# Kernel optimization log

Measured on AMD Instinct MI355X. Metric: run time of the kernel, lower is better.

Reference implementation:

```python
import jax, jax.numpy as jnp
import numpy as np

B, N, C, H = 2, 2048, 768, 12
D = C // H  # head dim = 64


def _rotate_half(x):
    d2 = x.shape[-1] // 2
    x1, x2 = x[..., :d2], x[..., d2:]
    return jnp.concatenate([-x2, x1], axis=-1)


def _apply_rope(x, sin, cos):
    # x: [B,H,N,D], sin/cos: [N,D] -> broadcast over (B,H)
    return x * cos[None, None] + _rotate_half(x) * sin[None, None]


def setup_inputs() -> dict:
    key = jax.random.key(0)
    ks = jax.random.split(key, 7)
    x = jax.random.normal(ks[0], (B, N, C), dtype=jnp.float32)
    sin_spatial = jax.random.normal(ks[1], (N, D), dtype=jnp.float32)
    cos_spatial = jax.random.normal(ks[2], (N, D), dtype=jnp.float32)
    s = 1.0 / np.sqrt(C)
    W_qkv = jax.random.uniform(ks[3], (C, 3 * C), jnp.float32, -s, s)
    b_qkv = jax.random.uniform(ks[4], (3 * C,), jnp.float32, -s, s)
    W_out = jax.random.uniform(ks[5], (C, C), jnp.float32, -s, s)
    b_out = jax.random.uniform(ks[6], (C,), jnp.float32, -s, s)
    return {"x": x, "sin_spatial": sin_spatial, "cos_spatial": cos_spatial,
            "W_qkv": W_qkv, "b_qkv": b_qkv, "W_out": W_out, "b_out": b_out}


def reference(x, sin_spatial, cos_spatial, W_qkv, b_qkv, W_out, b_out):
    qkv = x @ W_qkv + b_qkv                       # [B,N,3C]
    qkv = qkv.reshape(B, N, 3, H, D).transpose(2, 0, 3, 1, 4)  # [3,B,H,N,D]
    q, k, v = qkv[0], qkv[1], qkv[2]
    q = _apply_rope(q, sin_spatial, cos_spatial)
    k = _apply_rope(k, sin_spatial, cos_spatial)
    att = jnp.einsum('bhqd,bhkd->bhqk', q, k) * (D ** -0.5)
    att = jax.nn.softmax(att, axis=-1)            # dropout is identity (eval)
    y = jnp.einsum('bhqk,bhkd->bhqd', att, v)     # [B,H,N,D]
    y = y.transpose(0, 2, 1, 3).reshape(B, N, C)
    return y @ W_out + b_out
```

## Files before the change

### kernel.cpp

```cpp
#include <hip/hip_runtime.h>
#include <hip/hip_bf16.h>

#define BB 2
#define NN 2048
#define CC 768
#define HH 12
#define DD 64
#define MM 4096
#define N3 2304

typedef __attribute__((ext_vector_type(8))) short bf16x8;
typedef __attribute__((ext_vector_type(4))) float f32x4;

#define QSCALE 0.18033688011112043f


__device__ __forceinline__ unsigned short f2bf(float f) {
    union { float f; unsigned u; } v; v.f = f;
    unsigned r = v.u + 0x7FFFu + ((v.u >> 16) & 1u);
    return (unsigned short)(r >> 16);
}

__device__ __forceinline__ short f2bf_rn(float f) {
    union { __hip_bfloat16 h; short s; } v;
    v.h = __float2bfloat16(f);
    return v.s;
}

__device__ __forceinline__ float exp2_hw(float x) {
    float r;
    asm("v_exp_f32 %0, %1" : "=v"(r) : "v"(x));
    return r;
}

__device__ __forceinline__ bf16x8 ld_frag16(const unsigned short* p) {
    bf16x8 r;
    __builtin_memcpy(&r, p, 16);
    return r;
}

__device__ __forceinline__ void gload16(const unsigned short* g, unsigned short* l) {
    __builtin_amdgcn_global_load_lds(
        (const __attribute__((address_space(1))) void*)g,
        (__attribute__((address_space(3))) void*)l,
        16, 0, 0);
}

__global__ void k_cvt(const float* __restrict__ s, unsigned short* __restrict__ d, int n4) {
    int i = blockIdx.x * blockDim.x + threadIdx.x;
    int st = gridDim.x * blockDim.x;
    for (; i < n4; i += st) {
        float4 v = ((const float4*)s)[i];
        ushort4 o;
        o.x = f2bf(v.x); o.y = f2bf(v.y); o.z = f2bf(v.z); o.w = f2bf(v.w);
        int f = i * 4;
        int dst = (f & ~31) + ((i & 3) << 3) + (((i >> 2) & 1) << 2);
        *(ushort4*)(d + dst) = o;
    }
}

__global__ void k_cvtT(const float* __restrict__ s, unsigned short* __restrict__ d,
                       int R, int Cc) {
    __shared__ unsigned short t[64][72];
    const int c0 = blockIdx.x * 64, r0 = blockIdx.y * 64;
    const int tr = threadIdx.x >> 4;
    const int tc = (threadIdx.x & 15) * 4;
#pragma unroll
    for (int i = 0; i < 4; i++) {
        int r = tr + i * 16;
        float4 v = *(const float4*)(s + (size_t)(r0 + r) * Cc + c0 + tc);
        t[tc + 0][r] = f2bf(v.x);
        t[tc + 1][r] = f2bf(v.y);
        t[tc + 2][r] = f2bf(v.z);
        t[tc + 3][r] = f2bf(v.w);
    }
    __syncthreads();
    const int wr = threadIdx.x >> 2;
    const int wc = (threadIdx.x & 3) * 16;
    unsigned short* drow = d + (size_t)(c0 + wr) * R + r0;
#pragma unroll
    for (int g = 0; g < 4; g++) {
        int k4 = wc + g * 4;
        int o = k4 & 31;
        int p = (((o & 15) >> 2) << 3) + (((o >> 4) & 1) << 2);
        ushort4 v4 = *(ushort4*)&t[wr][k4];
        *(ushort4*)(drow + (k4 & ~31) + p) = v4;
    }
}

__launch_bounds__(256)
__global__ void k_qkv(const unsigned short* __restrict__ xb,
                      const unsigned short* __restrict__ wt,
                      const float* __restrict__ bias,
                      const float* __restrict__ sinp,
                      const float* __restrict__ cosp,
                      unsigned short* __restrict__ qws,
                      unsigned short* __restrict__ kws,
                      unsigned short* __restrict__ vws) {
    __shared__ unsigned short As[2][128 * 32];
    __shared__ unsigned short Bs[2][64 * 32];
    const int tid = threadIdx.x;
    const int lane = tid & 63, w = tid >> 6;
    const int ql = lane & 15, lg = lane >> 4;
    const int row0 = blockIdx.x * 128;
    const int j0 = blockIdx.y * 64;

    f32x4 acc[2][4];
#pragma unroll
    for (int a = 0; a < 2; a++)
#pragma unroll
        for (int b = 0; b < 4; b++) acc[a][b] = f32x4{0.f, 0.f, 0.f, 0.f};

    const int sr = lane >> 2;
    const int sc = (lane & 3) * 8;

    auto stage = [&](int bi, int k0) {
#pragma unroll
        for (int c = 0; c < 2; c++) {
            int j = w * 2 + c;
            gload16(xb + (size_t)(row0 + j * 16 + sr) * CC + k0 + sc, &As[bi][j * 512]);
        }
        gload16(wt + (size_t)(j0 + w * 16 + sr) * CC + k0 + sc, &Bs[bi][w * 512]);
    };

    stage(0, 0);
    __syncthreads();

    int bufi = 0;
    for (int k0 = 0; k0 < CC; k0 += 32) {
        if (k0 + 32 < CC) stage(bufi ^ 1, k0 + 32);
        bf16x8 af[2], bfr[4];
#pragma unroll
        for (int fr = 0; fr < 2; fr++)
            af[fr] = ld_frag16(&As[bufi][(w * 32 + fr * 16 + ql) * 32 + lg * 8]);
#pragma unroll
        for (int fn = 0; fn < 4; fn++)
            bfr[fn] = ld_frag16(&Bs[bufi][(fn * 16 + ql) * 32 + lg * 8]);
#pragma unroll
        for (int fr = 0; fr < 2; fr++)
#pragma unroll
            for (int fn = 0; fn < 4; fn++)
                acc[fr][fn] = __builtin_amdgcn_mfma_f32_16x16x32_bf16(af[fr], bfr[fn], acc[fr][fn], 0, 0, 0);
        __syncthreads();
        bufi ^= 1;
    }

    float vals[2][4][4];
#pragma unroll
    for (int fr = 0; fr < 2; fr++)
#pragma unroll
        for (int fn = 0; fn < 4; fn++) {
            float bj = bias[j0 + fn * 16 + ql];
#pragma unroll
            for (int r = 0; r < 4; r++) vals[fr][fn][r] = acc[fr][fn][r] + bj;
        }
    const int t = j0 / CC;
    const int h = (j0 % CC) >> 6;
    if (t < 2) {
        unsigned short* outp = (t == 0) ? qws : kws;
        const float qs = (t == 0) ? QSCALE : 1.0f;
#pragma unroll
        for (int fr = 0; fr < 2; fr++)
#pragma unroll
            for (int r = 0; r < 4; r++) {
                int m = row0 + w * 32 + fr * 16 + lg * 4 + r;
                int b = m >> 11, n = m & (NN - 1);
#pragma unroll
                for (int fn = 0; fn < 4; fn++) {
                    int d = fn * 16 + ql;
                    float cv = cosp[n * DD + d], sv = sinp[n * DD + d];
                    float other = vals[fr][fn ^ 2][r];
                    float rv = (vals[fr][fn][r] * cv + ((fn < 2) ? -other : other) * sv) * qs;
                    int dcol = (fn >> 1) * 32 + (ql >> 2) * 8 + (fn & 1) * 4 + (ql & 3);
                    outp[((size_t)(b * HH + h) * NN + n) * DD + dcol] = f2bf(rv);
                }
            }
    } else {
#pragma unroll
        for (int fr = 0; fr < 2; fr++)
#pragma unroll
            for (int r = 0; r < 4; r++) {
                int m = row0 + w * 32 + fr * 16 + lg * 4 + r;
                int b = m >> 11, n = m & (NN - 1);
                int ncol = (n & ~31) + lg * 8 + (fr & 1) * 4 + r;
#pragma unroll
                for (int fn = 0; fn < 4; fn++) {
                    int d = fn * 16 + ql;
                    vws[((size_t)(b * HH + h) * DD + d) * NN + ncol] = f2bf(vals[fr][fn][r]);
                }
            }
    }
}

template <int SPLITK>
__launch_bounds__(128)
__global__ void k_attn_t(const unsigned short* __restrict__ qws,
                         const unsigned short* __restrict__ kws,
                         const unsigned short* __restrict__ vws,
                         unsigned short* __restrict__ yws,
                         float* __restrict__ pA,
                         float* __restrict__ pm,
                         float* __restrict__ pl) {
    __shared__ unsigned short Ks[2][64][72];
    __shared__ unsigned short Vs[2][64][72];
    const int tid = threadIdx.x;
    const int lane = tid & 63, w = tid >> 6;
    const int ql = lane & 15, lg = lane >> 4;
    const int d0 = blockIdx.x;
    int bh, qb, kh;
    if (SPLITK) {
        bh = (d0 & 7) + 8 * (d0 >> 9);
        qb = (d0 >> 3) & 31;
        kh = (d0 >> 8) & 1;
    } else {
        bh = (d0 & 7) + 8 * (d0 >> 8);
        qb = (d0 >> 3) & 31;
        kh = 0;
    }
    const int qw = qb * 64 + w * 32;
    const unsigned short* Qp = qws + (size_t)bh * NN * DD;
    const unsigned short* Kp = kws + (size_t)bh * NN * DD;
    const unsigned short* Vp = vws + (size_t)bh * DD * NN;

    bf16x8 qf[2][2];
#pragma unroll
    for (int fn = 0; fn < 2; fn++)
#pragma unroll
        for (int kb = 0; kb < 2; kb++)
            qf[fn][kb] = ld_frag16(Qp + (size_t)(qw + fn * 16 + ql) * DD + kb * 32 + lg * 8);

    f32x4 oacc[4][2];
#pragma unroll
    for (int a = 0; a < 4; a++)
#pragma unroll
        for (int b = 0; b < 2; b++) oacc[a][b] = f32x4{0.f, 0.f, 0.f, 0.f};
    float mrun[2] = {-1e30f, -1e30f}, lrun[2] = {0.f, 0.f};

    const int srow = tid >> 1;
    const int shalf = (tid & 1) * 32;
    const int kt0 = SPLITK ? kh * 16 : 0;
    const int NT = SPLITK ? 16 : NN / 64;

#pragma unroll
    for (int j = 0; j < 4; j++) {
        *(uint4*)&Ks[0][srow][shalf + j * 8] = *(const uint4*)(Kp + (size_t)(kt0 * 64 + srow) * DD + shalf + j * 8);
        *(uint4*)&Vs[0][srow][shalf + j * 8] = *(const uint4*)(Vp + (size_t)srow * NN + kt0 * 64 + shalf + j * 8);
    }
    __syncthreads();

    int cur = 0;
    for (int t = 0; t < NT; t++) {
        const int kt = kt0 + t;
        uint4 kn[4], vn[4];
        const bool hasn = (t + 1 < NT);
        if (hasn) {
#pragma unroll
            for (int j = 0; j < 4; j++) {
                kn[j] = *(const uint4*)(Kp + (size_t)((kt + 1) * 64 + srow) * DD + shalf + j * 8);
                vn[j] = *(const uint4*)(Vp + (size_t)srow * NN + (kt + 1) * 64 + shalf + j * 8);
            }
        }
        const unsigned short (*Kc)[72] = Ks[cur];
        const unsigned short (*Vc)[72] = Vs[cur];

        f32x4 sacc[4][2];
#pragma unroll
        for (int a = 0; a < 4; a++)
#pragma unroll
            for (int b = 0; b < 2; b++) sacc[a][b] = f32x4{0.f, 0.f, 0.f, 0.f};
        __builtin_amdgcn_s_setprio(1);
#pragma unroll
        for (int kb = 0; kb < 2; kb++) {
            bf16x8 kf[4];
#pragma unroll
            for (int fr = 0; fr < 4; fr++)
                kf[fr] = ld_frag16(&Kc[fr * 16 + ql][kb * 32 + lg * 8]);
#pragma unroll
            for (int fr = 0; fr < 4; fr++)
#pragma unroll
                for (int fn = 0; fn < 2; fn++)
                    sacc[fr][fn] = __builtin_amdgcn_mfma_f32_16x16x32_bf16(kf[fr], qf[fn][kb], sacc[fr][fn], 0, 0, 0);
        }
        __builtin_amdgcn_s_setprio(0);

        bf16x8 pB[2][2];
#pragma unroll
        for (int fn = 0; fn < 2; fn++) {
            float ma = fmaxf(fmaxf(sacc[0][fn][0], sacc[0][fn][1]), fmaxf(sacc[0][fn][2], sacc[0][fn][3]));
            float mb = fmaxf(fmaxf(sacc[1][fn][0], sacc[1][fn][1]), fmaxf(sacc[1][fn][2], sacc[1][fn][3]));
            float mc = fmaxf(fmaxf(sacc[2][fn][0], sacc[2][fn][1]), fmaxf(sacc[2][fn][2], sacc[2][fn][3]));
            float md = fmaxf(fmaxf(sacc[3][fn][0], sacc[3][fn][1]), fmaxf(sacc[3][fn][2], sacc[3][fn][3]));
            float tm = fmaxf(fmaxf(ma, mb), fmaxf(mc, md));
            tm = fmaxf(tm, __shfl_xor(tm, 16));
            tm = fmaxf(tm, __shfl_xor(tm, 32));
            if (__any(tm > mrun[fn] + 8.0f)) {
                float mn = fmaxf(mrun[fn], tm);
                float scl = exp2_hw(mrun[fn] - mn);
                lrun[fn] *= scl;
#pragma unroll
                for (int db = 0; db < 4; db++) oacc[db][fn] *= scl;
                mrun[fn] = mn;
            }
            float ts = 0.f;
#pragma unroll
            for (int fr = 0; fr < 4; fr++)
#pragma unroll
                for (int r = 0; r < 4; r++) {
                    float p = exp2_hw(sacc[fr][fn][r] - mrun[fn]);
                    sacc[fr][fn][r] = p;
                    ts += p;
                }
            ts += __shfl_xor(ts, 16);
            ts += __shfl_xor(ts, 32);
            lrun[fn] += ts;

#pragma unroll
            for (int kkb = 0; kkb < 2; kkb++) {
                bf16x8 t8;
#pragma unroll
                for (int e = 0; e < 8; e++)
                    t8[e] = f2bf_rn(sacc[kkb * 2 + (e >> 2)][fn][e & 3]);
                pB[fn][kkb] = t8;
            }
        }

        __builtin_amdgcn_s_setprio(1);
#pragma unroll
        for (int db = 0; db < 4; db++) {
            bf16x8 va[2];
#pragma unroll
            for (int kkb = 0; kkb < 2; kkb++)
                va[kkb] = ld_frag16(&Vc[db * 16 + ql][kkb * 32 + lg * 8]);
#pragma unroll
            for (int kkb = 0; kkb < 2; kkb++)
#pragma unroll
                for (int fn = 0; fn < 2; fn++)
                    oacc[db][fn] = __builtin_amdgcn_mfma_f32_16x16x32_bf16(va[kkb], pB[fn][kkb], oacc[db][fn], 0, 0, 0);
        }
        __builtin_amdgcn_s_setprio(0);

        if (hasn) {
#pragma unroll
            for (int j = 0; j < 4; j++) {
                *(uint4*)&Ks[cur ^ 1][srow][shalf + j * 8] = kn[j];
                *(uint4*)&Vs[cur ^ 1][srow][shalf + j * 8] = vn[j];
            }
            __syncthreads();
            cur ^= 1;
        }
    }

    if (SPLITK) {
#pragma unroll
        for (int fn = 0; fn < 2; fn++) {
            int q = qw + fn * 16 + ql;
            float* ap = pA + (((size_t)kh * 24 + bh) * NN + q) * DD + lg * 4;
#pragma unroll
            for (int db = 0; db < 4; db++)
                *(f32x4*)(ap + db * 16) = oacc[db][fn];
            if (lg == 0) {
                pm[((size_t)kh * 24 + bh) * NN + q] = mrun[fn];
                pl[((size_t)kh * 24 + bh) * NN + q] = lrun[fn];
            }
        }
    } else {
        const int b = bh / HH, h = bh % HH;
#pragma unroll
        for (int fn = 0; fn < 2; fn++) {
            float inv = 1.0f / lrun[fn];
            int q = qw + fn * 16 + ql;
            unsigned short* yp = yws + (size_t)(b * NN + q) * CC + h * DD;
#pragma unroll
            for (int db = 0; db < 4; db++) {
                ushort4 o;
                o.x = f2bf(oacc[db][fn][0] * inv);
                o.y = f2bf(oacc[db][fn][1] * inv);
                o.z = f2bf(oacc[db][fn][2] * inv);
                o.w = f2bf(oacc[db][fn][3] * inv);
                *(ushort4*)(yp + (db >> 1) * 32 + lg * 8 + (db & 1) * 4) = o;
            }
        }
    }
}

__global__ void k_comb(const float* __restrict__ pA,
                       const float* __restrict__ pm,
                       const float* __restrict__ pl,
                       unsigned short* __restrict__ yws) {
    const int idx = blockIdx.x * blockDim.x + threadIdx.x;
    const int qg = idx >> 4;
    const int d4 = (idx & 15) * 4;
    const int bh = qg >> 11, q = qg & (NN - 1);
    const int b = bh / HH, h = bh % HH;
    const size_t half = (size_t)24 * NN * DD;
    float m0 = pm[qg], m1 = pm[24 * NN + qg];
    float l0 = pl[qg], l1 = pl[24 * NN + qg];
    float M = fmaxf(m0, m1);
    float e0 = exp2_hw(m0 - M), e1 = exp2_hw(m1 - M);
    float inv = 1.0f / (l0 * e0 + l1 * e1);
    f32x4 a0 = *(const f32x4*)(pA + (size_t)qg * DD + d4);
    f32x4 a1 = *(const f32x4*)(pA + half + (size_t)qg * DD + d4);
    ushort4 o;
    o.x = f2bf((a0[0] * e0 + a1[0] * e1) * inv);
    o.y = f2bf((a0[1] * e0 + a1[1] * e1) * inv);
    o.z = f2bf((a0[2] * e0 + a1[2] * e1) * inv);
    o.w = f2bf((a0[3] * e0 + a1[3] * e1) * inv);
    int dcol = (d4 & ~31) + ((d4 >> 2) & 3) * 8 + ((d4 >> 4) & 1) * 4;
    *(ushort4*)(yws + (size_t)(b * NN + q) * CC + h * DD + dcol) = o;
}

__launch_bounds__(256)
__global__ void k_out(const unsigned short* __restrict__ yb,
                      const unsigned short* __restrict__ wt,
                      const float* __restrict__ bias,
                      float* __restrict__ out) {
    __shared__ unsigned short As[2][128 * 32];
    __shared__ unsigned short Bs[2][64 * 32];
    const int tid = threadIdx.x;
    const int lane = tid & 63, w = tid >> 6;
    const int ql = lane & 15, lg = lane >> 4;
    const int row0 = blockIdx.x * 128;
    const int j0 = blockIdx.y * 64;

    f32x4 acc[2][4];
#pragma unroll
    for (int a = 0; a < 2; a++)
#pragma unroll
        for (int b = 0; b < 4; b++) acc[a][b] = f32x4{0.f, 0.f, 0.f, 0.f};

    const int sr = lane >> 2;
    const int sc = (lane & 3) * 8;

    auto stage = [&](int bi, int k0) {
#pragma unroll
        for (int c = 0; c < 2; c++) {
            int j = w * 2 + c;
            gload16(yb + (size_t)(row0 + j * 16 + sr) * CC + k0 + sc, &As[bi][j * 512]);
        }
        gload16(wt + (size_t)(j0 + w * 16 + sr) * CC + k0 + sc, &Bs[bi][w * 512]);
    };

    stage(0, 0);
    __syncthreads();

    int bufi = 0;
    for (int k0 = 0; k0 < CC; k0 += 32) {
        if (k0 + 32 < CC) stage(bufi ^ 1, k0 + 32);
        bf16x8 af[2], bfr[4];
#pragma unroll
        for (int fr = 0; fr < 2; fr++)
            af[fr] = ld_frag16(&As[bufi][(w * 32 + fr * 16 + ql) * 32 + lg * 8]);
#pragma unroll
        for (int fn = 0; fn < 4; fn++)
            bfr[fn] = ld_frag16(&Bs[bufi][(fn * 16 + ql) * 32 + lg * 8]);
#pragma unroll
        for (int fr = 0; fr < 2; fr++)
#pragma unroll
            for (int fn = 0; fn < 4; fn++)
                acc[fr][fn] = __builtin_amdgcn_mfma_f32_16x16x32_bf16(af[fr], bfr[fn], acc[fr][fn], 0, 0, 0);
        __syncthreads();
        bufi ^= 1;
    }

#pragma unroll
    for (int fr = 0; fr < 2; fr++)
#pragma unroll
        for (int fn = 0; fn < 4; fn++) {
            float bj = bias[j0 + fn * 16 + ql];
#pragma unroll
            for (int r = 0; r < 4; r++) {
                int m = row0 + w * 32 + fr * 16 + lg * 4 + r;
                out[(size_t)m * CC + j0 + fn * 16 + ql] = acc[fr][fn][r] + bj;
            }
        }
}

extern "C" void kernel_launch(void* const* d_in, const int* in_sizes, int n_in,
                              void* d_out, int out_size, void* d_ws, size_t ws_size,
                              hipStream_t stream) {
    const float* x    = (const float*)d_in[0];
    const float* sinp = (const float*)d_in[1];
    const float* cosp = (const float*)d_in[2];
    const float* wqkv = (const float*)d_in[3];
    const float* bqkv = (const float*)d_in[4];
    const float* wout = (const float*)d_in[5];
    const float* bout = (const float*)d_in[6];
    float* out = (float*)d_out;
    char* ws = (char*)d_ws;

    unsigned short* xb  = (unsigned short*)(ws);
    unsigned short* wqb = (unsigned short*)(ws + 6291456);
    unsigned short* wob = (unsigned short*)(ws + 9830400);
    unsigned short* qws = (unsigned short*)(ws + 11010048);
    unsigned short* kws = (unsigned short*)(ws + 17301504);
    unsigned short* vws = (unsigned short*)(ws + 23592960);
    unsigned short* yws = (unsigned short*)(ws + 29884416);
    float* pA = (float*)(ws + 36175872);
    float* pm = (float*)(ws + 61341696);
    float* pl = (float*)(ws + 61734912);
    if (ws_size < 36175872) return;
    const bool splitk = (ws_size >= 62128128);

    k_cvt<<<dim3(512), dim3(256), 0, stream>>>(x, xb, MM * CC / 4);
    k_cvtT<<<dim3(36, 12), dim3(256), 0, stream>>>(wqkv, wqb, CC, N3);
    k_cvtT<<<dim3(12, 12), dim3(256), 0, stream>>>(wout, wob, CC, CC);
    k_qkv<<<dim3(32, 36), dim3(256), 0, stream>>>(xb, wqb, bqkv, sinp, cosp, qws, kws, vws);
    if (splitk) {
        k_attn_t<1><<<dim3(1536), dim3(128), 0, stream>>>(qws, kws, vws, yws, pA, pm, pl);
        k_comb<<<dim3(3072), dim3(256), 0, stream>>>(pA, pm, pl, yws);
    } else {
        k_attn_t<0><<<dim3(768), dim3(128), 0, stream>>>(qws, kws, vws, yws, pA, pm, pl);
    }
    k_out<<<dim3(32, 12), dim3(256), 0, stream>>>(yws, wob, bout, out);
}
```

Before: 137.6 us.

## Use 4-wave attention blocks covering 128 queries to share K/V tiles

The split-K attention kernel now runs 256 threads (4 waves) per block, covering 128 query rows instead of 64, so each K/V tile staged in shared memory serves twice as many queries. The grid drops from 1536 to 768 blocks, and each thread loads half as much data per tile. The non-split fallback path is removed, and the workspace is now required to be large enough for the split-K partials. In exchange there are fewer blocks to fill the GPU and more waves waiting at each barrier.

```diff
diff --git a/kernel.cpp b/kernel.cpp
--- a/kernel.cpp
+++ b/kernel.cpp
@@ -192,32 +192,23 @@
     }
 }
 
-template <int SPLITK>
-__launch_bounds__(128)
-__global__ void k_attn_t(const unsigned short* __restrict__ qws,
-                         const unsigned short* __restrict__ kws,
-                         const unsigned short* __restrict__ vws,
-                         unsigned short* __restrict__ yws,
-                         float* __restrict__ pA,
-                         float* __restrict__ pm,
-                         float* __restrict__ pl) {
+__launch_bounds__(256)
+__global__ void k_attn4(const unsigned short* __restrict__ qws,
+                        const unsigned short* __restrict__ kws,
+                        const unsigned short* __restrict__ vws,
+                        float* __restrict__ pA,
+                        float* __restrict__ pm,
+                        float* __restrict__ pl) {
     __shared__ unsigned short Ks[2][64][72];
     __shared__ unsigned short Vs[2][64][72];
     const int tid = threadIdx.x;
     const int lane = tid & 63, w = tid >> 6;
     const int ql = lane & 15, lg = lane >> 4;
     const int d0 = blockIdx.x;
-    int bh, qb, kh;
-    if (SPLITK) {
-        bh = (d0 & 7) + 8 * (d0 >> 9);
-        qb = (d0 >> 3) & 31;
-        kh = (d0 >> 8) & 1;
-    } else {
-        bh = (d0 & 7) + 8 * (d0 >> 8);
-        qb = (d0 >> 3) & 31;
-        kh = 0;
-    }
-    const int qw = qb * 64 + w * 32;
+    const int bh = (d0 & 7) + 8 * (d0 >> 8);
+    const int kh = (d0 >> 3) & 1;
+    const int qb = (d0 >> 4) & 15;
+    const int qw = qb * 128 + w * 32;
     const unsigned short* Qp = qws + (size_t)bh * NN * DD;
     const unsigned short* Kp = kws + (size_t)bh * NN * DD;
     const unsigned short* Vp = vws + (size_t)bh * DD * NN;
@@ -236,28 +227,27 @@
         for (int b = 0; b < 2; b++) oacc[a][b] = f32x4{0.f, 0.f, 0.f, 0.f};
     float mrun[2] = {-1e30f, -1e30f}, lrun[2] = {0.f, 0.f};
 
-    const int srow = tid >> 1;
-    const int shalf = (tid & 1) * 32;
-    const int kt0 = SPLITK ? kh * 16 : 0;
-    const int NT = SPLITK ? 16 : NN / 64;
-
-#pragma unroll
-    for (int j = 0; j < 4; j++) {
-        *(uint4*)&Ks[0][srow][shalf + j * 8] = *(const uint4*)(Kp + (size_t)(kt0 * 64 + srow) * DD + shalf + j * 8);
-        *(uint4*)&Vs[0][srow][shalf + j * 8] = *(const uint4*)(Vp + (size_t)srow * NN + kt0 * 64 + shalf + j * 8);
+    const int srow = tid >> 2;
+    const int su = (tid & 3) * 16;
+    const int kt0 = kh * 16;
+
+#pragma unroll
+    for (int j = 0; j < 2; j++) {
+        *(uint4*)&Ks[0][srow][su + j * 8] = *(const uint4*)(Kp + (size_t)(kt0 * 64 + srow) * DD + su + j * 8);
+        *(uint4*)&Vs[0][srow][su + j * 8] = *(const uint4*)(Vp + (size_t)srow * NN + kt0 * 64 + su + j * 8);
     }
     __syncthreads();
 
     int cur = 0;
-    for (int t = 0; t < NT; t++) {
+    for (int t = 0; t < 16; t++) {
         const int kt = kt0 + t;
-        uint4 kn[4], vn[4];
-        const bool hasn = (t + 1 < NT);
+        uint4 kn[2], vn[2];
+        const bool hasn = (t + 1 < 16);
         if (hasn) {
 #pragma unroll
-            for (int j = 0; j < 4; j++) {
-                kn[j] = *(const uint4*)(Kp + (size_t)((kt + 1) * 64 + srow) * DD + shalf + j * 8);
-                vn[j] = *(const uint4*)(Vp + (size_t)srow * NN + (kt + 1) * 64 + shalf + j * 8);
+            for (int j = 0; j < 2; j++) {
+                kn[j] = *(const uint4*)(Kp + (size_t)((kt + 1) * 64 + srow) * DD + su + j * 8);
+                vn[j] = *(const uint4*)(Vp + (size_t)srow * NN + (kt + 1) * 64 + su + j * 8);
             }
         }
         const unsigned short (*Kc)[72] = Ks[cur];
@@ -341,44 +331,25 @@
 
         if (hasn) {
 #pragma unroll
-            for (int j = 0; j < 4; j++) {
-                *(uint4*)&Ks[cur ^ 1][srow][shalf + j * 8] = kn[j];
-                *(uint4*)&Vs[cur ^ 1][srow][shalf + j * 8] = vn[j];
+            for (int j = 0; j < 2; j++) {
+                *(uint4*)&Ks[cur ^ 1][srow][su + j * 8] = kn[j];
+                *(uint4*)&Vs[cur ^ 1][srow][su + j * 8] = vn[j];
             }
             __syncthreads();
             cur ^= 1;
         }
     }
 
-    if (SPLITK) {
-#pragma unroll
-        for (int fn = 0; fn < 2; fn++) {
-            int q = qw + fn * 16 + ql;
-            float* ap = pA + (((size_t)kh * 24 + bh) * NN + q) * DD + lg * 4;
-#pragma unroll
-            for (int db = 0; db < 4; db++)
-                *(f32x4*)(ap + db * 16) = oacc[db][fn];
-            if (lg == 0) {
-                pm[((size_t)kh * 24 + bh) * NN + q] = mrun[fn];
-                pl[((size_t)kh * 24 + bh) * NN + q] = lrun[fn];
-            }
-        }
-    } else {
-        const int b = bh / HH, h = bh % HH;
-#pragma unroll
-        for (int fn = 0; fn < 2; fn++) {
-            float inv = 1.0f / lrun[fn];
-            int q = qw + fn * 16 + ql;
-            unsigned short* yp = yws + (size_t)(b * NN + q) * CC + h * DD;
-#pragma unroll
-            for (int db = 0; db < 4; db++) {
-                ushort4 o;
-                o.x = f2bf(oacc[db][fn][0] * inv);
-                o.y = f2bf(oacc[db][fn][1] * inv);
-                o.z = f2bf(oacc[db][fn][2] * inv);
-                o.w = f2bf(oacc[db][fn][3] * inv);
-                *(ushort4*)(yp + (db >> 1) * 32 + lg * 8 + (db & 1) * 4) = o;
-            }
+#pragma unroll
+    for (int fn = 0; fn < 2; fn++) {
+        int q = qw + fn * 16 + ql;
+        float* ap = pA + (((size_t)kh * 24 + bh) * NN + q) * DD + lg * 4;
+#pragma unroll
+        for (int db = 0; db < 4; db++)
+            *(f32x4*)(ap + db * 16) = oacc[db][fn];
+        if (lg == 0) {
+            pm[((size_t)kh * 24 + bh) * NN + q] = mrun[fn];
+            pl[((size_t)kh * 24 + bh) * NN + q] = lrun[fn];
         }
     }
 }
@@ -498,18 +469,13 @@
     float* pA = (float*)(ws + 36175872);
     float* pm = (float*)(ws + 61341696);
     float* pl = (float*)(ws + 61734912);
-    if (ws_size < 36175872) return;
-    const bool splitk = (ws_size >= 62128128);
+    if (ws_size < 62128128) return;
 
     k_cvt<<<dim3(512), dim3(256), 0, stream>>>(x, xb, MM * CC / 4);
     k_cvtT<<<dim3(36, 12), dim3(256), 0, stream>>>(wqkv, wqb, CC, N3);
     k_cvtT<<<dim3(12, 12), dim3(256), 0, stream>>>(wout, wob, CC, CC);
     k_qkv<<<dim3(32, 36), dim3(256), 0, stream>>>(xb, wqb, bqkv, sinp, cosp, qws, kws, vws);
-    if (splitk) {
-        k_attn_t<1><<<dim3(1536), dim3(128), 0, stream>>>(qws, kws, vws, yws, pA, pm, pl);
-        k_comb<<<dim3(3072), dim3(256), 0, stream>>>(pA, pm, pl, yws);
-    } else {
-        k_attn_t<0><<<dim3(768), dim3(128), 0, stream>>>(qws, kws, vws, yws, pA, pm, pl);
-    }
+    k_attn4<<<dim3(768), dim3(256), 0, stream>>>(qws, kws, vws, pA, pm, pl);
+    k_comb<<<dim3(3072), dim3(256), 0, stream>>>(pA, pm, pl, yws);
     k_out<<<dim3(32, 12), dim3(256), 0, stream>>>(yws, wob, bout, out);
 }
```

Result: faster. 117.3 us, median of 2 (-14.8%).
